# Optimization experiments

Measured on AMD Instinct MI355X. Metric: run time of the kernel, lower is better.

## Reference

```python
import jax, jax.numpy as jnp
import numpy as np

D = 256      # d_model
H = 8        # nhead
L = 6        # num_layers
FF = 1024    # dim_feedforward
S = 64       # 8x8 board squares
HD = D // H  # head dim


def make_pe():
    # Faithful to PositionalEncoding loops: pe[i,j,k]=sin(i/10000**(k/C)) for even k,
    # pe[i,j,k+1]=cos(j/10000**(k/C)). Flattened to [64, D] in (i*8+j) token order.
    i = jnp.arange(8.0)[:, None, None]          # row index
    j = jnp.arange(8.0)[None, :, None]          # col index
    k_even = jnp.arange(0, D, 2, dtype=jnp.float32)
    div = 10000.0 ** (k_even / D)               # [D/2]
    pe_even = jnp.sin(i / div) * jnp.ones((8, 8, D // 2))
    pe_odd = jnp.cos(j / div) * jnp.ones((8, 8, D // 2))
    pe = jnp.stack([pe_even, pe_odd], axis=-1).reshape(8, 8, D)
    return pe.reshape(S, D)


def layer_norm(x, g, b, eps=1e-5):
    m = jnp.mean(x, axis=-1, keepdims=True)
    v = jnp.mean(jnp.square(x - m), axis=-1, keepdims=True)
    return (x - m) * jax.lax.rsqrt(v + eps) * g + b


def setup_inputs() -> dict:
    key = jax.random.key(0)
    ks = iter(jax.random.split(key, 40))
    s = 0.02
    B = 4096
    inp = {
        'board_tensor': jax.random.normal(next(ks), (B, 14, 8, 8), jnp.float32),
        'emb': jax.random.normal(next(ks), (15, D)) * s,
        'qkv_w': jax.random.normal(next(ks), (L, 3 * D, D)) * s,
        'qkv_b': jnp.zeros((L, 3 * D)),
        'out_w': jax.random.normal(next(ks), (L, D, D)) * s,
        'out_b': jnp.zeros((L, D)),
        'ln1_g': jnp.ones((L, D)), 'ln1_b': jnp.zeros((L, D)),
        'ln2_g': jnp.ones((L, D)), 'ln2_b': jnp.zeros((L, D)),
        'ff1_w': jax.random.normal(next(ks), (L, FF, D)) * s,
        'ff1_b': jnp.zeros((L, FF)),
        'ff2_w': jax.random.normal(next(ks), (L, D, FF)) * s,
        'ff2_b': jnp.zeros((L, D)),
        'vw1': jax.random.normal(next(ks), (256, D)) * s, 'vb1': jnp.zeros((256,)),
        'vw2': jax.random.normal(next(ks), (1, 256)) * s, 'vb2': jnp.zeros((1,)),
        'pw1': jax.random.normal(next(ks), (1024, D * S)) * s, 'pb1': jnp.zeros((1024,)),
        'pw2': jax.random.normal(next(ks), (4096, 1024)) * s, 'pb2': jnp.zeros((4096,)),
        'cw1': jax.random.normal(next(ks), (256, D)) * s, 'cb1': jnp.zeros((256,)),
        'cw2': jax.random.normal(next(ks), (3, 256)) * s, 'cb2': jnp.zeros((3,)),
    }
    return inp


def reference(board_tensor, emb, qkv_w, qkv_b, out_w, out_b, ln1_g, ln1_b,
              ln2_g, ln2_b, ff1_w, ff1_b, ff2_w, ff2_b, vw1, vb1, vw2, vb2,
              pw1, pb1, pw2, pb2, cw1, cb1, cw2, cb2):
    B = board_tensor.shape[0]
    # vectorized board_to_tokens: argmax over piece channels per square
    cells = board_tensor.transpose(0, 2, 3, 1).reshape(B, S, 14)  # [B,64,14]
    idx = jnp.argmax(cells, axis=-1)
    mx = jnp.max(cells, axis=-1)
    tokens = jnp.where(mx > 0, idx + 1, 0)  # [B,64] int

    x = emb[tokens] + make_pe()  # [B,64,D]

    scale = 1.0 / jnp.sqrt(jnp.float32(HD))
    for l in range(L):
        qkv = x @ qkv_w[l].T + qkv_b[l]                 # [B,S,3D]
        q, k, v = jnp.split(qkv, 3, axis=-1)
        q = q.reshape(B, S, H, HD)
        k = k.reshape(B, S, H, HD)
        v = v.reshape(B, S, H, HD)
        scores = jnp.einsum('bqhd,bkhd->bhqk', q, k) * scale
        attn = jax.nn.softmax(scores, axis=-1)
        o = jnp.einsum('bhqk,bkhd->bqhd', attn, v).reshape(B, S, D)
        o = o @ out_w[l].T + out_b[l]
        x = layer_norm(x + o, ln1_g[l], ln1_b[l])       # post-norm
        ff = jax.nn.relu(x @ ff1_w[l].T + ff1_b[l]) @ ff2_w[l].T + ff2_b[l]
        x = layer_norm(x + ff, ln2_g[l], ln2_b[l])

    pooled = jnp.mean(x, axis=1)                        # [B,D]
    value = jnp.tanh(jax.nn.relu(pooled @ vw1.T + vb1) @ vw2.T + vb2)
    policy = jax.nn.relu(x.reshape(B, -1) @ pw1.T + pb1) @ pw2.T + pb2
    classification = jax.nn.relu(pooled @ cw1.T + cb1) @ cw2.T + cb2
    return (value, policy, classification)
```

## Files before the change

### kernel.cpp

```cpp
#include <hip/hip_runtime.h>
#include <math.h>

#define BB 4096
#define SEQ 64
#define DM 256
#define NH 8
#define HDIM 32
#define NL 6
#define FFD 1024
#define NT (BB*SEQ)

typedef __attribute__((ext_vector_type(8))) short bf16x8;
typedef __attribute__((ext_vector_type(4))) float f32x4;
typedef __attribute__((ext_vector_type(8))) unsigned short u16x8;

__device__ __forceinline__ unsigned short f2bf(float f) {
  unsigned u = __float_as_uint(f);
  unsigned r = u + 0x7FFFu + ((u >> 16) & 1u);
  return (unsigned short)(r >> 16);
}
__device__ __forceinline__ float bf2f(unsigned short h) {
  return __uint_as_float(((unsigned)h) << 16);
}
__device__ __forceinline__ void gload_lds16(const void* g, void* l) {
  __builtin_amdgcn_global_load_lds((const __attribute__((address_space(1))) unsigned*)g,
                                   (__attribute__((address_space(3))) unsigned*)l, 16, 0, 0);
}

__global__ void pe_kernel(float* __restrict__ pe) {
  int g = blockIdx.x * 256 + threadIdx.x;
  if (g >= SEQ * DM) return;
  int s = g >> 8, d = g & 255;
  int i = s >> 3, j = s & 7;
  float ex = (float)(d & ~1) * (1.0f / DM);
  float dv = powf(10000.0f, ex);
  pe[g] = (d & 1) ? cosf((float)j / dv) : sinf((float)i / dv);
}

__global__ void tok_kernel(const float* __restrict__ board, int* __restrict__ toks) {
  int n = blockIdx.x * 256 + threadIdx.x;
  if (n >= NT) return;
  int b = n >> 6, s = n & 63;
  const float* p = board + (size_t)b * (14 * 64) + s;
  float mx = p[0]; int idx = 0;
#pragma unroll
  for (int c = 1; c < 14; ++c) {
    float v = p[(size_t)c * 64];
    if (v > mx) { mx = v; idx = c; }
  }
  toks[n] = (mx > 0.0f) ? idx + 1 : 0;
}

__global__ void cvt_kernel(const float* __restrict__ src, unsigned short* __restrict__ dst, int n4) {
  int g = blockIdx.x * 256 + threadIdx.x;
  if (g >= n4) return;
  float4 v = *(const float4*)(src + (size_t)g * 4);
  ushort4 r;
  r.x = f2bf(v.x); r.y = f2bf(v.y); r.z = f2bf(v.z); r.w = f2bf(v.w);
  *(ushort4*)(dst + (size_t)g * 4) = r;
}

__global__ void embed_kernel(const int* __restrict__ toks, const float* __restrict__ emb,
                             const float* __restrict__ pe, float* __restrict__ x,
                             unsigned short* __restrict__ xbf, int cnt) {
  int g = blockIdx.x * 256 + threadIdx.x;
  if (g >= cnt * (DM / 4)) return;
  int n = g >> 6, q = g & 63;
  int s = n & 63;
  int tok = toks[n];
  float4 e = *(const float4*)(emb + (size_t)tok * DM + q * 4);
  float4 p = *(const float4*)(pe + (size_t)s * DM + q * 4);
  float4 r; r.x = e.x + p.x; r.y = e.y + p.y; r.z = e.z + p.z; r.w = e.w + p.w;
  *(float4*)(x + (size_t)n * DM + q * 4) = r;
  ushort4 h; h.x = f2bf(r.x); h.y = f2bf(r.y); h.z = f2bf(r.z); h.w = f2bf(r.w);
  *(ushort4*)(xbf + (size_t)n * DM + q * 4) = h;
}

template<bool OUTBF, bool RELU, bool BIAS>
__global__ __launch_bounds__(256) void gemm_bf16(
    const unsigned short* __restrict__ A, const unsigned short* __restrict__ W,
    const float* __restrict__ bias, void* __restrict__ Cout,
    int M, int N, int K)
{
  __shared__ __align__(16) short As[128 * 64];
  __shared__ __align__(16) short Bs[128 * 64];
  const int bm = blockIdx.x * 128;
  const int bn = blockIdx.y * 128;
  const int tid = threadIdx.x;
  const int lane = tid & 63;
  const int wave = tid >> 6;
  const int wr = wave >> 1, wc = wave & 1;
  const int lo16 = lane & 15, hi4 = lane >> 4;

  const int tr = tid >> 3;
  const int sc_lin = tid & 7;
  const int arow = wr * 64 + lo16;
  const int brow = wc * 64 + lo16;
  const int amask = (arow & 7) << 4;
  const int bmask = (brow & 7) << 4;

  f32x4 acc[4][4];
#pragma unroll
  for (int m = 0; m < 4; ++m)
#pragma unroll
    for (int n = 0; n < 4; ++n) acc[m][n] = (f32x4)0.f;

  const char* Asc = (const char*)As;
  const char* Bsc = (const char*)Bs;
  char* AsW = (char*)As + (tid & 192) * 16;
  char* BsW = (char*)Bs + (tid & 192) * 16;

  for (int k0 = 0; k0 < K; k0 += 64) {
#pragma unroll
    for (int i = 0; i < 4; ++i) {
      int row = tr + i * 32;
      int sc = sc_lin ^ (row & 7);
      gload_lds16(A + (size_t)(bm + row) * K + k0 + sc * 8, AsW + i * 4096);
      gload_lds16(W + (size_t)(bn + row) * K + k0 + sc * 8, BsW + i * 4096);
    }
    __syncthreads();
#pragma unroll
    for (int kk = 0; kk < 2; ++kk) {
      const int colb = kk * 64 + hi4 * 16;
      bf16x8 av[4], bv[4];
#pragma unroll
      for (int m = 0; m < 4; ++m)
        av[m] = *(const bf16x8*)(Asc + (arow + m * 16) * 128 + (colb ^ amask));
#pragma unroll
      for (int n = 0; n < 4; ++n)
        bv[n] = *(const bf16x8*)(Bsc + (brow + n * 16) * 128 + (colb ^ bmask));
#pragma unroll
      for (int m = 0; m < 4; ++m)
#pragma unroll
        for (int n = 0; n < 4; ++n)
          acc[m][n] = __builtin_amdgcn_mfma_f32_16x16x32_bf16(av[m], bv[n], acc[m][n], 0, 0, 0);
    }
    __syncthreads();
  }

#pragma unroll
  for (int n = 0; n < 4; ++n) {
    const int col = bn + wc * 64 + n * 16 + lo16;
    const float bv = BIAS ? bias[col] : 0.f;
#pragma unroll
    for (int m = 0; m < 4; ++m) {
      const int rowb = bm + wr * 64 + m * 16 + hi4 * 4;
#pragma unroll
      for (int j = 0; j < 4; ++j) {
        float v = acc[m][n][j] + bv;
        if (RELU) v = fmaxf(v, 0.f);
        if (OUTBF) ((unsigned short*)Cout)[(size_t)(rowb + j) * N + col] = f2bf(v);
        else       ((float*)Cout)[(size_t)(rowb + j) * N + col] = v;
      }
    }
  }
}

__global__ __launch_bounds__(64) void attn_kernel(const unsigned short* __restrict__ qkv,
                                                  unsigned short* __restrict__ o) {
  __shared__ float Ks[64][32];
  __shared__ float Vs[64][32];
  int bh = blockIdx.x;
  int b = bh >> 3, h = bh & 7;
  int t = threadIdx.x;
  const size_t base = (size_t)b * 64 * 768 + (size_t)h * 32;

  int rq = t >> 2;
  int cq = (t & 3) * 8;
#pragma unroll
  for (int p = 0; p < 4; ++p) {
    int r = p * 16 + rq;
    u16x8 kv = *(const u16x8*)(qkv + base + (size_t)r * 768 + 256 + cq);
    u16x8 vv = *(const u16x8*)(qkv + base + (size_t)r * 768 + 512 + cq);
#pragma unroll
    for (int j = 0; j < 8; ++j) { Ks[r][cq + j] = bf2f(kv[j]); Vs[r][cq + j] = bf2f(vv[j]); }
  }
  float q[32];
#pragma unroll
  for (int c = 0; c < 4; ++c) {
    u16x8 qv = *(const u16x8*)(qkv + base + (size_t)t * 768 + c * 8);
#pragma unroll
    for (int j = 0; j < 8; ++j) q[c * 8 + j] = bf2f(qv[j]);
  }
  __syncthreads();

  const float scale = 0.17677669529663687f;
  float sc[64];
#pragma unroll
  for (int jr = 0; jr < 64; ++jr) {
    float s = 0.f;
#pragma unroll
    for (int d = 0; d < 32; ++d) s += q[d] * Ks[jr][d];
    sc[jr] = s * scale;
  }
  float m = sc[0];
#pragma unroll
  for (int jr = 1; jr < 64; ++jr) m = fmaxf(m, sc[jr]);
  float sum = 0.f;
#pragma unroll
  for (int jr = 0; jr < 64; ++jr) { sc[jr] = expf(sc[jr] - m); sum += sc[jr]; }
  float inv = 1.f / sum;

  float oa[32];
#pragma unroll
  for (int d = 0; d < 32; ++d) oa[d] = 0.f;
#pragma unroll
  for (int jr = 0; jr < 64; ++jr) {
    float p = sc[jr];
#pragma unroll
    for (int d = 0; d < 32; ++d) oa[d] += p * Vs[jr][d];
  }
  unsigned short* op = o + (size_t)(b * 64 + t) * DM + h * 32;
#pragma unroll
  for (int c = 0; c < 4; ++c) {
    u16x8 r;
#pragma unroll
    for (int j = 0; j < 8; ++j) r[j] = f2bf(oa[c * 8 + j] * inv);
    *(u16x8*)(op + c * 8) = r;
  }
}

__global__ __launch_bounds__(256) void ln_kernel(const float* __restrict__ xin,
                                                 const float* __restrict__ delta,
                                                 const float* __restrict__ g,
                                                 const float* __restrict__ beta,
                                                 float* __restrict__ xout,
                                                 unsigned short* __restrict__ xbf, int nrows) {
  int row = (blockIdx.x * 256 + threadIdx.x) >> 6;
  int lane = threadIdx.x & 63;
  if (row >= nrows) return;
  float4 xv = *(const float4*)(xin + (size_t)row * DM + lane * 4);
  float4 dv = *(const float4*)(delta + (size_t)row * DM + lane * 4);
  float v0 = xv.x + dv.x, v1 = xv.y + dv.y, v2 = xv.z + dv.z, v3 = xv.w + dv.w;
  float s1 = v0 + v1 + v2 + v3;
  float s2 = v0 * v0 + v1 * v1 + v2 * v2 + v3 * v3;
#pragma unroll
  for (int off = 32; off; off >>= 1) {
    s1 += __shfl_xor(s1, off);
    s2 += __shfl_xor(s2, off);
  }
  float mean = s1 * (1.f / DM);
  float var = s2 * (1.f / DM) - mean * mean;
  float r = rsqrtf(var + 1e-5f);
  float4 gv = *(const float4*)(g + lane * 4);
  float4 bv = *(const float4*)(beta + lane * 4);
  float4 outv;
  outv.x = (v0 - mean) * r * gv.x + bv.x;
  outv.y = (v1 - mean) * r * gv.y + bv.y;
  outv.z = (v2 - mean) * r * gv.z + bv.z;
  outv.w = (v3 - mean) * r * gv.w + bv.w;
  *(float4*)(xout + (size_t)row * DM + lane * 4) = outv;
  ushort4 h; h.x = f2bf(outv.x); h.y = f2bf(outv.y); h.z = f2bf(outv.z); h.w = f2bf(outv.w);
  *(ushort4*)(xbf + (size_t)row * DM + lane * 4) = h;
}

template<bool BIAS, bool RELU>
__global__ __launch_bounds__(256) void gemm_f32(
    const float* __restrict__ A, const float* __restrict__ W,
    const float* __restrict__ bias, float* __restrict__ C,
    int M, int N, int K)
{
  __shared__ float As[32][68];
  __shared__ float Bs[32][68];
  const int bm = blockIdx.x * 64;
  const int bn = blockIdx.y * 64;
  const int tid = threadIdx.x;
  const int lr = tid >> 3;
  const int lc = (tid & 7) * 4;
  const int ty = tid >> 4;
  const int tx = tid & 15;
  float acc[4][4] = {{0.f}};

  for (int k0 = 0; k0 < K; k0 += 32) {
#pragma unroll
    for (int p = 0; p < 2; ++p) {
      int r = lr + p * 32;
      float4 av = *(const float4*)(A + (size_t)(bm + r) * K + k0 + lc);
      As[lc + 0][r] = av.x; As[lc + 1][r] = av.y; As[lc + 2][r] = av.z; As[lc + 3][r] = av.w;
      float4 wv = *(const float4*)(W + (size_t)(bn + r) * K + k0 + lc);
      Bs[lc + 0][r] = wv.x; Bs[lc + 1][r] = wv.y; Bs[lc + 2][r] = wv.z; Bs[lc + 3][r] = wv.w;
    }
    __syncthreads();
#pragma unroll
    for (int k = 0; k < 32; ++k) {
      float4 a = *(const float4*)&As[k][ty * 4];
      float4 b = *(const float4*)&Bs[k][tx * 4];
      acc[0][0] += a.x * b.x; acc[0][1] += a.x * b.y; acc[0][2] += a.x * b.z; acc[0][3] += a.x * b.w;
      acc[1][0] += a.y * b.x; acc[1][1] += a.y * b.y; acc[1][2] += a.y * b.z; acc[1][3] += a.y * b.w;
      acc[2][0] += a.z * b.x; acc[2][1] += a.z * b.y; acc[2][2] += a.z * b.z; acc[2][3] += a.z * b.w;
      acc[3][0] += a.w * b.x; acc[3][1] += a.w * b.y; acc[3][2] += a.w * b.z; acc[3][3] += a.w * b.w;
    }
    __syncthreads();
  }

  float4 bv = make_float4(0.f, 0.f, 0.f, 0.f);
  if (BIAS) bv = *(const float4*)(bias + bn + tx * 4);
#pragma unroll
  for (int i = 0; i < 4; ++i) {
    float4 r;
    r.x = acc[i][0] + bv.x; r.y = acc[i][1] + bv.y;
    r.z = acc[i][2] + bv.z; r.w = acc[i][3] + bv.w;
    if (RELU) {
      r.x = fmaxf(r.x, 0.f); r.y = fmaxf(r.y, 0.f);
      r.z = fmaxf(r.z, 0.f); r.w = fmaxf(r.w, 0.f);
    }
    *(float4*)(C + (size_t)(bm + ty * 4 + i) * N + bn + tx * 4) = r;
  }
}

__global__ void pool_kernel(const float* __restrict__ x, float* __restrict__ pooled, int nb) {
  int g = blockIdx.x * 256 + threadIdx.x;
  if (g >= nb * DM) return;
  int b = g >> 8, d = g & 255;
  const float* p = x + (size_t)b * SEQ * DM + d;
  float s = 0.f;
#pragma unroll
  for (int t = 0; t < SEQ; ++t) s += p[(size_t)t * DM];
  pooled[g] = s * (1.f / SEQ);
}

__global__ void value_kernel(const float* __restrict__ h, const float* __restrict__ w,
                             const float* __restrict__ bias, float* __restrict__ out, int nb) {
  int row = (blockIdx.x * 256 + threadIdx.x) >> 6;
  int lane = threadIdx.x & 63;
  if (row >= nb) return;
  float4 hv = *(const float4*)(h + (size_t)row * DM + lane * 4);
  float4 wv = *(const float4*)(w + lane * 4);
  float s = hv.x * wv.x + hv.y * wv.y + hv.z * wv.z + hv.w * wv.w;
#pragma unroll
  for (int off = 32; off; off >>= 1) s += __shfl_xor(s, off);
  if (lane == 0) out[row] = tanhf(s + bias[0]);
}

__global__ void cls_kernel(const float* __restrict__ h, const float* __restrict__ w,
                           const float* __restrict__ bias, float* __restrict__ out, int nb) {
  int row = (blockIdx.x * 256 + threadIdx.x) >> 6;
  int lane = threadIdx.x & 63;
  if (row >= nb) return;
  float4 hv = *(const float4*)(h + (size_t)row * DM + lane * 4);
#pragma unroll
  for (int j = 0; j < 3; ++j) {
    float4 wv = *(const float4*)(w + (size_t)j * DM + lane * 4);
    float s = hv.x * wv.x + hv.y * wv.y + hv.z * wv.z + hv.w * wv.w;
#pragma unroll
    for (int off = 32; off; off >>= 1) s += __shfl_xor(s, off);
    if (lane == 0) out[(size_t)row * 3 + j] = s + bias[j];
  }
}

extern "C" void kernel_launch(void* const* d_in, const int* in_sizes, int n_in,
                              void* d_out, int out_size, void* d_ws, size_t ws_size,
                              hipStream_t stream) {
  const float* board = (const float*)d_in[0];
  const float* emb   = (const float*)d_in[1];
  const float* qkv_w = (const float*)d_in[2];
  const float* qkv_b = (const float*)d_in[3];
  const float* out_w = (const float*)d_in[4];
  const float* out_b = (const float*)d_in[5];
  const float* ln1_g = (const float*)d_in[6];
  const float* ln1_b = (const float*)d_in[7];
  const float* ln2_g = (const float*)d_in[8];
  const float* ln2_b = (const float*)d_in[9];
  const float* ff1_w = (const float*)d_in[10];
  const float* ff1_b = (const float*)d_in[11];
  const float* ff2_w = (const float*)d_in[12];
  const float* ff2_b = (const float*)d_in[13];
  const float* vw1 = (const float*)d_in[14];
  const float* vb1 = (const float*)d_in[15];
  const float* vw2 = (const float*)d_in[16];
  const float* vb2 = (const float*)d_in[17];
  const float* pw1 = (const float*)d_in[18];
  const float* pb1 = (const float*)d_in[19];
  const float* pw2 = (const float*)d_in[20];
  const float* pb2 = (const float*)d_in[21];
  const float* cw1 = (const float*)d_in[22];
  const float* cb1 = (const float*)d_in[23];
  const float* cw2 = (const float*)d_in[24];
  const float* cb2 = (const float*)d_in[25];
  (void)in_sizes; (void)n_in; (void)out_size;

  char* ws = (char*)d_ws;
  float* pe       = (float*)(ws + 0);
  int*   toks_all = (int*)  (ws + 65536);
  unsigned short* qkvw_bf = (unsigned short*)(ws + 1114112);
  unsigned short* outw_bf = (unsigned short*)(ws + 3473408);
  unsigned short* ff1w_bf = (unsigned short*)(ws + 4259840);
  unsigned short* ff2w_bf = (unsigned short*)(ws + 7405568);
  unsigned short* pw1_bf  = (unsigned short*)(ws + 10551296);
  unsigned short* pw2_bf  = (unsigned short*)(ws + 44105728);
  const size_t header = 52494336;

  int CB = 2048;
  while (CB > 128 && header + (size_t)CB * 64 * 6656 > ws_size) CB >>= 1;
  const int NCH = BB / CB;
  const int CNT = CB * SEQ;

  float*          x_c    = (float*)(ws + header);
  unsigned short* x_bf   = (unsigned short*)(x_c + (size_t)CNT * DM);
  unsigned short* qkv_bf = x_bf + (size_t)CNT * DM;
  unsigned short* o_bf   = qkv_bf + (size_t)CNT * 768;
  unsigned short* mid_bf = o_bf + (size_t)CNT * DM;
  float*          delta  = (float*)(mid_bf + (size_t)CNT * FFD);
  float*          pooled = delta;
  unsigned short* ph_bf  = mid_bf;
  float*          vh     = (float*)qkv_bf;
  float*          chb    = vh + (size_t)CB * DM;

  float* out = (float*)d_out;
  float* value_out  = out;
  float* policy_out = out + BB;
  float* cls_out    = out + BB + (size_t)BB * 4096;

  pe_kernel<<<64, 256, 0, stream>>>(pe);
  tok_kernel<<<NT / 256, 256, 0, stream>>>(board, toks_all);

  cvt_kernel<<<(6*768*256/4 + 255)/256, 256, 0, stream>>>(qkv_w, qkvw_bf, 6*768*256/4);
  cvt_kernel<<<(6*256*256/4 + 255)/256, 256, 0, stream>>>(out_w, outw_bf, 6*256*256/4);
  cvt_kernel<<<(6*1024*256/4 + 255)/256, 256, 0, stream>>>(ff1_w, ff1w_bf, 6*1024*256/4);
  cvt_kernel<<<(6*256*1024/4 + 255)/256, 256, 0, stream>>>(ff2_w, ff2w_bf, 6*256*1024/4);
  cvt_kernel<<<(1024*16384/4 + 255)/256, 256, 0, stream>>>(pw1, pw1_bf, 1024*16384/4);
  cvt_kernel<<<(4096*1024/4 + 255)/256, 256, 0, stream>>>(pw2, pw2_bf, 4096*1024/4);

  for (int c = 0; c < NCH; ++c) {
    const int b0 = c * CB;
    const int* toks_c = toks_all + (size_t)b0 * SEQ;

    embed_kernel<<<CNT / 4, 256, 0, stream>>>(toks_c, emb, pe, x_c, x_bf, CNT);

    for (int l = 0; l < NL; ++l) {
      gemm_bf16<true, false, true><<<dim3(CNT/128, 768/128), 256, 0, stream>>>(
          x_bf, qkvw_bf + (size_t)l * 768 * DM, qkv_b + (size_t)l * 768, qkv_bf, CNT, 768, DM);
      attn_kernel<<<CB * NH, 64, 0, stream>>>(qkv_bf, o_bf);
      gemm_bf16<false, false, true><<<dim3(CNT/128, DM/128), 256, 0, stream>>>(
          o_bf, outw_bf + (size_t)l * DM * DM, out_b + (size_t)l * DM, delta, CNT, DM, DM);
      ln_kernel<<<CNT / 4, 256, 0, stream>>>(x_c, delta, ln1_g + (size_t)l * DM,
                                             ln1_b + (size_t)l * DM, x_c, x_bf, CNT);
      gemm_bf16<true, true, true><<<dim3(CNT/128, FFD/128), 256, 0, stream>>>(
          x_bf, ff1w_bf + (size_t)l * FFD * DM, ff1_b + (size_t)l * FFD, mid_bf, CNT, FFD, DM);
      gemm_bf16<false, false, true><<<dim3(CNT/128, DM/128), 256, 0, stream>>>(
          mid_bf, ff2w_bf + (size_t)l * DM * FFD, ff2_b + (size_t)l * DM, delta, CNT, DM, FFD);
      ln_kernel<<<CNT / 4, 256, 0, stream>>>(x_c, delta, ln2_g + (size_t)l * DM,
                                             ln2_b + (size_t)l * DM, x_c, x_bf, CNT);
    }

    pool_kernel<<<CB, 256, 0, stream>>>(x_c, pooled, CB);

    gemm_f32<true, true><<<dim3(CB / 64, DM / 64), 256, 0, stream>>>(
        pooled, vw1, vb1, vh, CB, DM, DM);
    value_kernel<<<CB / 4, 256, 0, stream>>>(vh, vw2, vb2, value_out + b0, CB);

    gemm_bf16<true, true, true><<<dim3(CB/128, FFD/128), 256, 0, stream>>>(
        x_bf, pw1_bf, pb1, ph_bf, CB, FFD, DM * SEQ);
    gemm_bf16<false, false, true><<<dim3(CB/128, 4096/128), 256, 0, stream>>>(
        ph_bf, pw2_bf, pb2, policy_out + (size_t)b0 * 4096, CB, 4096, FFD);

    gemm_f32<true, true><<<dim3(CB / 64, DM / 64), 256, 0, stream>>>(
        pooled, cw1, cb1, chb, CB, DM, DM);
    cls_kernel<<<CB / 4, 256, 0, stream>>>(chb, cw2, cb2, cls_out + (size_t)b0 * 3, CB);
  }
}
```

Measured before the change: 16.99 ms.

## Double-buffer LDS tiles in bf16 GEMM to overlap global loads with MFMA

The GEMM now uses two LDS buffers per operand. It issues the next K-tile's global-to-LDS loads before computing on the current tile and waits with a partial vmcnt, so memory latency can overlap with MFMA work. This doubles LDS use to 64KB per block, which may reduce occupancy. It also relies on hand-written s_waitcnt counts matching the eight outstanding loads per stage.

```diff
diff --git a/kernel.cpp b/kernel.cpp
--- a/kernel.cpp
+++ b/kernel.cpp
@@ -82,8 +82,8 @@
     const float* __restrict__ bias, void* __restrict__ Cout,
     int M, int N, int K)
 {
-  __shared__ __align__(16) short As[128 * 64];
-  __shared__ __align__(16) short Bs[128 * 64];
+  __shared__ __align__(16) short As[2][128 * 64];
+  __shared__ __align__(16) short Bs[2][128 * 64];
   const int bm = blockIdx.x * 128;
   const int bn = blockIdx.y * 128;
   const int tid = threadIdx.x;
@@ -98,6 +98,7 @@
   const int brow = wc * 64 + lo16;
   const int amask = (arow & 7) << 4;
   const int bmask = (brow & 7) << 4;
+  const int ldsW = (tid & 192) * 16;
 
   f32x4 acc[4][4];
 #pragma unroll
@@ -105,20 +106,33 @@
 #pragma unroll
     for (int n = 0; n < 4; ++n) acc[m][n] = (f32x4)0.f;
 
-  const char* Asc = (const char*)As;
-  const char* Bsc = (const char*)Bs;
-  char* AsW = (char*)As + (tid & 192) * 16;
-  char* BsW = (char*)Bs + (tid & 192) * 16;
-
-  for (int k0 = 0; k0 < K; k0 += 64) {
+  const int nk = K >> 6;
+
+  auto STAGE = [&](int buf, int k0) {
 #pragma unroll
     for (int i = 0; i < 4; ++i) {
       int row = tr + i * 32;
       int sc = sc_lin ^ (row & 7);
-      gload_lds16(A + (size_t)(bm + row) * K + k0 + sc * 8, AsW + i * 4096);
-      gload_lds16(W + (size_t)(bn + row) * K + k0 + sc * 8, BsW + i * 4096);
-    }
-    __syncthreads();
+      gload_lds16(A + (size_t)(bm + row) * K + k0 + sc * 8,
+                  (char*)As[buf] + ldsW + i * 4096);
+      gload_lds16(W + (size_t)(bn + row) * K + k0 + sc * 8,
+                  (char*)Bs[buf] + ldsW + i * 4096);
+    }
+  };
+
+  STAGE(0, 0);
+  for (int t = 0; t < nk; ++t) {
+    const int cur = t & 1;
+    if (t + 1 < nk) {
+      STAGE(cur ^ 1, (t + 1) << 6);
+      asm volatile("s_waitcnt vmcnt(8)" ::: "memory");
+    } else {
+      asm volatile("s_waitcnt vmcnt(0)" ::: "memory");
+    }
+    __builtin_amdgcn_s_barrier();
+
+    const char* Asc = (const char*)As[cur];
+    const char* Bsc = (const char*)Bs[cur];
 #pragma unroll
     for (int kk = 0; kk < 2; ++kk) {
       const int colb = kk * 64 + hi4 * 16;
@@ -135,7 +149,7 @@
         for (int n = 0; n < 4; ++n)
           acc[m][n] = __builtin_amdgcn_mfma_f32_16x16x32_bf16(av[m], bv[n], acc[m][n], 0, 0, 0);
     }
-    __syncthreads();
+    __builtin_amdgcn_s_barrier();
   }
 
 #pragma unroll
```

Measured after the change: 15.81 ms. -6.9%, faster.
